# Kernel optimization log

Hardware: AMD Instinct MI355X
Metric: run time of the kernel (lower is better)

The kernel has to match this reference:

```python
import jax, jax.numpy as jnp
import numpy as np

P = 64  # number of parameters per grid cell
# torch.combinations(param, 2, with_replacement=True) enumerates (i,j) with i<=j
# in row-major order, which matches np.triu_indices.
IDX_I, IDX_J = np.triu_indices(P)  # each length C = P*(P+1)//2 = 2080


def setup_inputs() -> dict:
    key = jax.random.key(0)
    k1, k2 = jax.random.split(key)
    # [B, G1, G2, P]
    param_tensor = jax.random.normal(k1, (32, 64, 64, P), dtype=jnp.float32)
    # [G1, G2, C]
    coeffs = jax.random.normal(k2, (64, 64, len(IDX_I)), dtype=jnp.float32)
    return {"param_tensor": param_tensor, "coeffs": coeffs}


def reference(param_tensor, coeffs):
    # Pairwise products with replacement: p_i * p_j for i <= j  -> [B,G1,G2,C]
    pair = param_tensor[..., IDX_I] * param_tensor[..., IDX_J]
    # Per-cell weighted sum over combinations, then sum over the 2D grid -> [B]
    cell = jnp.einsum('bijc,ijc->bij', pair, coeffs)
    return cell.sum(axis=(1, 2))
```

## Files before the change

kernel.cpp:

```cpp
#include <hip/hip_runtime.h>

#define NP     64
#define NC     2080
#define NCELLS 4096
#define NB     32
#define CELLS_PER_BLOCK 4
#define BLOCKS (NCELLS / CELLS_PER_BLOCK)

typedef short bf16x8 __attribute__((ext_vector_type(8)));
typedef float f32x16 __attribute__((ext_vector_type(16)));

__device__ __forceinline__ short f2bf(float f) {
  unsigned u = __float_as_uint(f);
  u += 0x7fffu + ((u >> 16) & 1u);
  return (short)(u >> 16);
}

__global__ __launch_bounds__(256, 2) void poly_mfma_kernel(
    const float* __restrict__ param,
    const float* __restrict__ coeffs,
    float* __restrict__ ws) {
  const int tid  = threadIdx.x;
  const int wave = tid >> 6;
  const int lane = tid & 63;
  const int lo5  = lane & 31;
  const int hi   = lane >> 5;
  const int cell = blockIdx.x * CELLS_PER_BLOCK + wave;

  const float* pb = param + ((size_t)lo5 * NCELLS + cell) * NP;
  bf16x8 afrag[4];
#pragma unroll
  for (int ks = 0; ks < 4; ++ks) {
#pragma unroll
    for (int eh = 0; eh < 2; ++eh) {
      const int i0 = ks * 16 + 4 * hi + 8 * eh;
      const float4 v = *reinterpret_cast<const float4*>(pb + i0);
      afrag[ks][eh * 4 + 0] = f2bf(v.x);
      afrag[ks][eh * 4 + 1] = f2bf(v.y);
      afrag[ks][eh * 4 + 2] = f2bf(v.z);
      afrag[ks][eh * 4 + 3] = f2bf(v.w);
    }
  }

  const float* cb = coeffs + (size_t)cell * NC;
  f32x16 acc0, acc1;
#pragma unroll
  for (int r = 0; r < 16; ++r) { acc0[r] = 0.f; acc1[r] = 0.f; }

#pragma unroll
  for (int ks = 0; ks < 4; ++ks) {
    bf16x8 b0, b1;
#pragma unroll
    for (int e = 0; e < 8; ++e) {
      const int i = ks * 16 + 4 * hi + (e & 3) + 8 * (e >> 2);
      const int cbase = i * (127 - i) / 2;
      const float v0 = (lo5 >= i) ? cb[cbase + lo5] : 0.f;
      const float v1 = (lo5 + 32 >= i) ? cb[cbase + lo5 + 32] : 0.f;
      b0[e] = f2bf(v0);
      b1[e] = f2bf(v1);
    }
    acc0 = __builtin_amdgcn_mfma_f32_32x32x16_bf16(afrag[ks], b0, acc0, 0, 0, 0);
    acc1 = __builtin_amdgcn_mfma_f32_32x32x16_bf16(afrag[ks], b1, acc1, 0, 0, 0);
  }

  float dacc[16];
#pragma unroll
  for (int r = 0; r < 16; ++r) {
    const int b = (r & 3) + 8 * (r >> 2) + 4 * hi;
    const float* pe = param + ((size_t)b * NCELLS + cell) * NP;
    dacc[r] = fmaf(acc0[r], pe[lo5], acc1[r] * pe[lo5 + 32]);
  }

#pragma unroll
  for (int r = 0; r < 16; ++r) {
    float v = dacc[r];
    v += __shfl_xor(v, 1, 64);
    v += __shfl_xor(v, 2, 64);
    v += __shfl_xor(v, 4, 64);
    v += __shfl_xor(v, 8, 64);
    v += __shfl_xor(v, 16, 64);
    dacc[r] = v;
  }

  __shared__ float sred[CELLS_PER_BLOCK][NB];
  if (lo5 == 0) {
#pragma unroll
    for (int r = 0; r < 16; ++r) {
      const int b = (r & 3) + 8 * (r >> 2) + 4 * hi;
      sred[wave][b] = dacc[r];
    }
  }
  __syncthreads();
  if (tid < NB) {
    ws[(size_t)blockIdx.x * NB + tid] =
        sred[0][tid] + sred[1][tid] + sred[2][tid] + sred[3][tid];
  }
}

__global__ void poly_reduce_kernel(const float* __restrict__ ws,
                                   float* __restrict__ out) {
  __shared__ float sred[8][NB];
  const int tid = threadIdx.x;
  const int b = tid & 31;
  const int part = tid >> 5;
  float s = 0.f;
  for (int k = 0; k < BLOCKS / 8; ++k) {
    s += ws[(size_t)(part * (BLOCKS / 8) + k) * NB + b];
  }
  sred[part][b] = s;
  __syncthreads();
  if (tid < NB) {
    float t = 0.f;
#pragma unroll
    for (int q = 0; q < 8; ++q) t += sred[q][tid];
    out[tid] = t;
  }
}

extern "C" void kernel_launch(void* const* d_in, const int* in_sizes, int n_in,
                              void* d_out, int out_size, void* d_ws,
                              size_t ws_size, hipStream_t stream) {
  const float* param = (const float*)d_in[0];
  const float* coeffs = (const float*)d_in[1];
  float* out = (float*)d_out;
  float* ws = (float*)d_ws;

  hipLaunchKernelGGL(poly_mfma_kernel, dim3(BLOCKS), dim3(256), 0, stream,
                     param, coeffs, ws);
  hipLaunchKernelGGL(poly_reduce_kernel, dim3(1), dim3(256), 0, stream, ws,
                     out);
}
```

Before: 26.16 us.

## Split each cell's column halves across two waves and vectorize the final reduction

Each grid cell's two 32-column MFMA halves now go to two separate waves instead of one wave doing both, so a block handles two cells with four waves. This halves per-wave work and accumulator registers and raises the occupancy hint, aiming to hide the latency of the scattered coefficient loads. The workspace is transposed to batch-major so the reduce kernel can read contiguous float4 runs. In exchange, the A fragment and param loads are duplicated across the paired waves, and the reduce kernel now sums twice as many partials.

After: 34.48 us. 31.8% more time.

```diff
diff --git a/kernel.cpp b/kernel.cpp
--- a/kernel.cpp
+++ b/kernel.cpp
@@ -4,7 +4,7 @@
 #define NC     2080
 #define NCELLS 4096
 #define NB     32
-#define CELLS_PER_BLOCK 4
+#define CELLS_PER_BLOCK 2
 #define BLOCKS (NCELLS / CELLS_PER_BLOCK)
 
 typedef short bf16x8 __attribute__((ext_vector_type(8)));
@@ -16,7 +16,7 @@
   return (short)(u >> 16);
 }
 
-__global__ __launch_bounds__(256, 2) void poly_mfma_kernel(
+__global__ __launch_bounds__(256, 6) void poly_mfma_kernel(
     const float* __restrict__ param,
     const float* __restrict__ coeffs,
     float* __restrict__ ws) {
@@ -25,7 +25,10 @@
   const int lane = tid & 63;
   const int lo5  = lane & 31;
   const int hi   = lane >> 5;
-  const int cell = blockIdx.x * CELLS_PER_BLOCK + wave;
+  const int cl   = wave >> 1;
+  const int jh   = wave & 1;
+  const int cell = blockIdx.x * CELLS_PER_BLOCK + cl;
+  const int jg   = 32 * jh + lo5;
 
   const float* pb = param + ((size_t)lo5 * NCELLS + cell) * NP;
   bf16x8 afrag[4];
@@ -43,34 +46,31 @@
   }
 
   const float* cb = coeffs + (size_t)cell * NC;
-  f32x16 acc0, acc1;
+  f32x16 acc;
 #pragma unroll
-  for (int r = 0; r < 16; ++r) { acc0[r] = 0.f; acc1[r] = 0.f; }
+  for (int r = 0; r < 16; ++r) acc[r] = 0.f;
 
 #pragma unroll
   for (int ks = 0; ks < 4; ++ks) {
-    bf16x8 b0, b1;
+    bf16x8 bfr;
 #pragma unroll
     for (int e = 0; e < 8; ++e) {
       const int i = ks * 16 + 4 * hi + (e & 3) + 8 * (e >> 2);
       const int cbase = i * (127 - i) / 2;
-      const float v0 = (lo5 >= i) ? cb[cbase + lo5] : 0.f;
-      const float v1 = (lo5 + 32 >= i) ? cb[cbase + lo5 + 32] : 0.f;
-      b0[e] = f2bf(v0);
-      b1[e] = f2bf(v1);
+      const float v = (jg >= i) ? cb[cbase + jg] : 0.f;
+      bfr[e] = f2bf(v);
     }
-    acc0 = __builtin_amdgcn_mfma_f32_32x32x16_bf16(afrag[ks], b0, acc0, 0, 0, 0);
-    acc1 = __builtin_amdgcn_mfma_f32_32x32x16_bf16(afrag[ks], b1, acc1, 0, 0, 0);
+    acc = __builtin_amdgcn_mfma_f32_32x32x16_bf16(afrag[ks], bfr, acc, 0, 0, 0);
   }
 
+  __shared__ float sred[4][NB];
   float dacc[16];
 #pragma unroll
   for (int r = 0; r < 16; ++r) {
     const int b = (r & 3) + 8 * (r >> 2) + 4 * hi;
     const float* pe = param + ((size_t)b * NCELLS + cell) * NP;
-    dacc[r] = fmaf(acc0[r], pe[lo5], acc1[r] * pe[lo5 + 32]);
+    dacc[r] = acc[r] * pe[jg];
   }
-
 #pragma unroll
   for (int r = 0; r < 16; ++r) {
     float v = dacc[r];
@@ -81,8 +81,6 @@
     v += __shfl_xor(v, 16, 64);
     dacc[r] = v;
   }
-
-  __shared__ float sred[CELLS_PER_BLOCK][NB];
   if (lo5 == 0) {
 #pragma unroll
     for (int r = 0; r < 16; ++r) {
@@ -92,27 +90,31 @@
   }
   __syncthreads();
   if (tid < NB) {
-    ws[(size_t)blockIdx.x * NB + tid] =
+    ws[(size_t)tid * BLOCKS + blockIdx.x] =
         sred[0][tid] + sred[1][tid] + sred[2][tid] + sred[3][tid];
   }
 }
 
 __global__ void poly_reduce_kernel(const float* __restrict__ ws,
                                    float* __restrict__ out) {
-  __shared__ float sred[8][NB];
+  __shared__ float sred[NB][8];
   const int tid = threadIdx.x;
-  const int b = tid & 31;
-  const int part = tid >> 5;
+  const int b = tid >> 3;
+  const int part = tid & 7;
+  const float4* src =
+      reinterpret_cast<const float4*>(ws + (size_t)b * BLOCKS + part * (BLOCKS / 8));
   float s = 0.f;
-  for (int k = 0; k < BLOCKS / 8; ++k) {
-    s += ws[(size_t)(part * (BLOCKS / 8) + k) * NB + b];
+#pragma unroll 4
+  for (int k = 0; k < BLOCKS / 8 / 4; ++k) {
+    float4 v = src[k];
+    s += (v.x + v.y) + (v.z + v.w);
   }
-  sred[part][b] = s;
+  sred[b][part] = s;
   __syncthreads();
   if (tid < NB) {
     float t = 0.f;
 #pragma unroll
-    for (int q = 0; q < 8; ++q) t += sred[q][tid];
+    for (int q = 0; q < 8; ++q) t += sred[tid][q];
     out[tid] = t;
   }
 }
```
